# Kernel optimization log

Measured on AMD Instinct MI355X. Metric: run time of the kernel, lower is better.

## Reference

```python
import jax, jax.numpy as jnp
import numpy as np

B, C, H, W = 2, 256, 32, 32
NUM_HEADS = 8
HEAD_DIM = C // NUM_HEADS
SCALE = HEAD_DIM ** -0.5
K1, K2 = 2, 3
KERNELS = [3, 5, 7]
STRIDES = [1, 1, 1]
PADS = [1, 2, 3]


def avgpool2d(y, k, s, p):
    # PyTorch AvgPool2d default count_include_pad=True: divide by k*k always
    yp = jnp.pad(y, ((0, 0), (0, 0), (p, p), (p, p)))
    summed = jax.lax.reduce_window(yp, 0.0, jax.lax.add,
                                   (1, 1, k, k), (1, 1, s, s), 'VALID')
    return summed / float(k * k)


def layer_norm(x, g, b, eps=1e-5):
    mu = jnp.mean(x, axis=-1, keepdims=True)
    var = jnp.var(x, axis=-1, keepdims=True)
    return (x - mu) / jnp.sqrt(var + eps) * g + b


def topk_mask(attn, kk):
    # boolean mask with True at the top-kk positions along the last axis
    idx = jax.lax.top_k(attn, kk)[1]                     # [B,h,N,kk]
    mask = jnp.zeros(attn.shape, dtype=bool)
    return jnp.put_along_axis(mask, idx, True, axis=-1, inplace=False)


def setup_inputs() -> dict:
    key = jax.random.key(0)
    ks = jax.random.split(key, 8)
    std = 1.0 / np.sqrt(C)
    return {
        'x': jax.random.normal(ks[0], (B, C, H, W), jnp.float32),
        'y': jax.random.normal(ks[1], (B, C, H, W), jnp.float32),
        'Wq': jax.random.uniform(ks[2], (C, C), jnp.float32, -std, std),
        'Wkv': jax.random.uniform(ks[3], (2 * C, C), jnp.float32, -std, std),
        'Wproj': jax.random.uniform(ks[4], (C, C), jnp.float32, -std, std),
        'bproj': jax.random.uniform(ks[5], (C,), jnp.float32, -std, std),
        'ln_g': jnp.ones((C,), jnp.float32),
        'ln_b': jnp.zeros((C,), jnp.float32),
        'attn1_p': jnp.full((1,), 0.5, jnp.float32),
        'attn2_p': jnp.full((1,), 0.5, jnp.float32),
    }


def reference(x, y, Wq, Wkv, Wproj, bproj, ln_g, ln_b, attn1_p, attn2_p):
    # multi-scale average pooling fusion of y (stride 1 keeps H,W)
    yf = (avgpool2d(y, KERNELS[0], STRIDES[0], PADS[0])
          + avgpool2d(y, KERNELS[1], STRIDES[1], PADS[1])
          + avgpool2d(y, KERNELS[2], STRIDES[2], PADS[2]))
    yf = yf.reshape(B, C, H * W).transpose(0, 2, 1)      # [B, N1, C]
    yf = layer_norm(yf, ln_g, ln_b)
    N1 = yf.shape[1]

    kv = yf @ Wkv.T                                      # [B, N1, 2C]
    kv = kv.reshape(B, N1, 2, NUM_HEADS, HEAD_DIM).transpose(2, 0, 3, 1, 4)
    k, v = kv[0], kv[1]                                  # [B, h, N1, d]

    xf = x.reshape(B, C, H * W).transpose(0, 2, 1)       # [B, N, C]
    N = xf.shape[1]
    q = (xf @ Wq.T).reshape(B, N, NUM_HEADS, HEAD_DIM).transpose(0, 2, 1, 3)

    attn = jnp.einsum('bhnd,bhmd->bhnm', q, k) * SCALE   # [B, h, N, N1]

    neg_inf = jnp.array(-jnp.inf, attn.dtype)
    m1 = topk_mask(attn, int(N1 / K1))
    a1 = jax.nn.softmax(jnp.where(m1, attn, neg_inf), axis=-1)
    out1 = jnp.einsum('bhnm,bhmd->bhnd', a1, v)

    m2 = topk_mask(attn, int(N1 / K2))
    a2 = jax.nn.softmax(jnp.where(m2, attn, neg_inf), axis=-1)
    out2 = jnp.einsum('bhnm,bhmd->bhnd', a2, v)

    out = out1 * attn1_p + out2 * attn2_p                # [B, h, N, d]
    out = out.transpose(0, 2, 1, 3).reshape(B, N, C)
    out = out @ Wproj.T + bproj
    hw = int(np.sqrt(N))
    return out.transpose(0, 2, 1).reshape(B, C, hw, hw)
```

## Files before the change

### kernel.cpp

```cpp
#include <hip/hip_runtime.h>

typedef _Float16 f16;
typedef f16 f16x8 __attribute__((ext_vector_type(8)));
typedef f16 f16x4 __attribute__((ext_vector_type(4)));
typedef float f32x4 __attribute__((ext_vector_type(4)));

constexpr float ATT_SCALE = 0.17677669529663687f;
constexpr float LOG2E = 1.4426950408889634f;

template<int C> __device__ __forceinline__ float dppadd(float v) {
    return v + __int_as_float(__builtin_amdgcn_update_dpp(0, __float_as_int(v), C, 0xf, 0xf, true));
}
template<int C> __device__ __forceinline__ float dppmax(float v) {
    return fmaxf(v, __int_as_float(__builtin_amdgcn_update_dpp(__float_as_int(v), __float_as_int(v), C, 0xf, 0xf, false)));
}
__device__ __forceinline__ float wave_sum(float v) {
    v = dppadd<0x111>(v); v = dppadd<0x112>(v); v = dppadd<0x114>(v); v = dppadd<0x118>(v);
    v = dppadd<0x142>(v); v = dppadd<0x143>(v);
    return __int_as_float(__builtin_amdgcn_readlane(__float_as_int(v), 63));
}
__device__ __forceinline__ float wave_max(float v) {
    v = dppmax<0x111>(v); v = dppmax<0x112>(v); v = dppmax<0x114>(v); v = dppmax<0x118>(v);
    v = dppmax<0x142>(v); v = dppmax<0x143>(v);
    return __int_as_float(__builtin_amdgcn_readlane(__float_as_int(v), 63));
}

__global__ __launch_bounds__(256) void prep_kernel(const float* __restrict__ y,
                                                   float* __restrict__ pooled,
                                                   const float* __restrict__ x,
                                                   f16* __restrict__ xT,
                                                   const float* __restrict__ Wq,
                                                   const float* __restrict__ Wkv,
                                                   const float* __restrict__ Wp,
                                                   const float* __restrict__ lng,
                                                   const float* __restrict__ lnb,
                                                   f16* __restrict__ wq16,
                                                   f16* __restrict__ wkv16,
                                                   f16* __restrict__ wp16,
                                                   float* __restrict__ sg,
                                                   float* __restrict__ sb)
{
    __shared__ float sh[1444];
    int bid = blockIdx.x, t = threadIdx.x;
    if (bid < 512) {
        float (*p)[38] = (float(*)[38])sh;
        const float* plane = y + (size_t)bid * 1024;
        for (int i = t; i < 38 * 38; i += 256) (&p[0][0])[i] = 0.f;
        __syncthreads();
        for (int i = t; i < 1024; i += 256) p[(i >> 5) + 3][(i & 31) + 3] = plane[i];
        __syncthreads();
        int b = bid >> 8, c = bid & 255;
        for (int i = t; i < 1024; i += 256) {
            int r = (i >> 5) + 3, cc = (i & 31) + 3;
            float s3 = 0.f;
            #pragma unroll
            for (int dr = -1; dr <= 1; ++dr)
                #pragma unroll
                for (int dc = -1; dc <= 1; ++dc) s3 += p[r + dr][cc + dc];
            float r5 = 0.f;
            #pragma unroll
            for (int dc = -2; dc <= 2; ++dc) r5 += p[r - 2][cc + dc] + p[r + 2][cc + dc];
            #pragma unroll
            for (int dr = -1; dr <= 1; ++dr) r5 += p[r + dr][cc - 2] + p[r + dr][cc + 2];
            float r7 = 0.f;
            #pragma unroll
            for (int dc = -3; dc <= 3; ++dc) r7 += p[r - 3][cc + dc] + p[r + 3][cc + dc];
            #pragma unroll
            for (int dr = -2; dr <= 2; ++dr) r7 += p[r + dr][cc - 3] + p[r + dr][cc + 3];
            float s5 = s3 + r5, s7 = s5 + r7;
            pooled[((size_t)b * 1024 + i) * 256 + c] =
                s3 * (1.f / 9.f) + s5 * (1.f / 25.f) + s7 * (1.f / 49.f);
        }
    } else if (bid < 1024) {
        float (*tile)[33] = (float(*)[33])sh;
        int id = bid - 512;
        int b = id >> 8, ct = (id >> 5) & 7, nt = id & 31;
        int rr = t >> 5, j = t & 31;
        #pragma unroll
        for (int r = rr; r < 32; r += 8)
            tile[r][j] = x[((size_t)b * 256 + ct * 32 + r) * 1024 + nt * 32 + j];
        __syncthreads();
        #pragma unroll
        for (int r = rr; r < 32; r += 8)
            xT[((size_t)b * 1024 + nt * 32 + r) * 256 + ct * 32 + j] = (f16)tile[j][r];
    } else if (bid < 1536) {
        int i = (bid - 1024) * 256 + t;
        if (i < 65536) { wq16[i] = (f16)Wq[i]; wp16[i] = (f16)Wp[i]; }
        wkv16[i] = (f16)(Wkv[i] * lng[i & 255]);
    } else {
        int o = (bid - 1536) * 256 + t;
        const float4* wr = (const float4*)(Wkv + (size_t)o * 256);
        const float4* gr = (const float4*)lng;
        const float4* br = (const float4*)lnb;
        float sgs = 0.f, sbs = 0.f;
        #pragma unroll 8
        for (int c4 = 0; c4 < 64; ++c4) {
            float4 wv = wr[c4], gv = gr[c4], bv = br[c4];
            sgs += wv.x * gv.x + wv.y * gv.y + wv.z * gv.z + wv.w * gv.w;
            sbs += wv.x * bv.x + wv.y * bv.y + wv.z * bv.z + wv.w * bv.w;
        }
        sg[o] = sgs; sb[o] = sbs;
    }
}

__device__ __forceinline__ void gemm_tile(const f16* __restrict__ A, const f16* __restrict__ Bm,
                                          int row0, int ncol0, int l15, int lhi, f32x4 acc[4])
{
    for (int k0 = 0; k0 < 256; k0 += 32) {
        f16x8 a = *(const f16x8*)(A + (size_t)(row0 + l15) * 256 + k0 + lhi * 8);
        #pragma unroll
        for (int j = 0; j < 4; ++j) {
            f16x8 bf = *(const f16x8*)(Bm + (size_t)(ncol0 + j * 16 + l15) * 256 + k0 + lhi * 8);
            acc[j] = __builtin_amdgcn_mfma_f32_16x16x32_f16(a, bf, acc[j], 0, 0, 0);
        }
    }
}

__global__ __launch_bounds__(256) void qkv_kernel(const f16* __restrict__ xT,
                                                  const float* __restrict__ pooled,
                                                  const f16* __restrict__ wq16,
                                                  const f16* __restrict__ wkv16,
                                                  const float* __restrict__ sg,
                                                  const float* __restrict__ sb,
                                                  f16* __restrict__ q16,
                                                  f16* __restrict__ k16,
                                                  f16* __restrict__ vT16)
{
    int w = threadIdx.x >> 6, lane = threadIdx.x & 63;
    int l15 = lane & 15, lhi = lane >> 4;
    if (blockIdx.x < 128) {
        int mt = blockIdx.x >> 2, nt = blockIdx.x & 3;
        int row0 = mt * 64 + w * 16;
        f32x4 acc[4] = {};
        gemm_tile(xT, wq16, row0, nt * 64, l15, lhi, acc);
        #pragma unroll
        for (int j = 0; j < 4; ++j) {
            int col = nt * 64 + j * 16 + l15;
            int h = col >> 5, d = col & 31;
            #pragma unroll
            for (int r = 0; r < 4; ++r) {
                int row = row0 + 4 * lhi + r;
                int b = row >> 10, n = row & 1023;
                q16[(((size_t)(b * 8 + h)) * 1024 + n) * 32 + d] = (f16)(acc[j][r] * ATT_SCALE);
            }
        }
    } else {
        __shared__ float st_part[64][4][2];
        __shared__ float stats[64][2];
        int bid = blockIdx.x - 128;
        int mt = bid >> 3, nt = bid & 7;
        int row0g = mt * 64;
        {
            int row = threadIdx.x >> 2, part = threadIdx.x & 3;
            const float4* pr = (const float4*)(pooled + (size_t)(row0g + row) * 256 + part * 64);
            float su = 0.f, qq = 0.f;
            #pragma unroll
            for (int i = 0; i < 16; ++i) {
                float4 v = pr[i];
                su += v.x + v.y + v.z + v.w;
                qq += v.x * v.x + v.y * v.y + v.z * v.z + v.w * v.w;
            }
            st_part[row][part][0] = su; st_part[row][part][1] = qq;
        }
        __syncthreads();
        if (threadIdx.x < 64) {
            int row = threadIdx.x;
            float su = st_part[row][0][0] + st_part[row][1][0] + st_part[row][2][0] + st_part[row][3][0];
            float qq = st_part[row][0][1] + st_part[row][1][1] + st_part[row][2][1] + st_part[row][3][1];
            float mu = su * (1.f / 256.f);
            float rstd = rsqrtf(qq * (1.f / 256.f) - mu * mu + 1e-5f);
            stats[row][0] = mu; stats[row][1] = rstd;
        }
        __syncthreads();
        f32x4 acc[4] = {};
        const float* Ap = pooled + (size_t)(row0g + w * 16 + l15) * 256;
        for (int k0 = 0; k0 < 256; k0 += 32) {
            float4 u0 = *(const float4*)(Ap + k0 + lhi * 8);
            float4 u1 = *(const float4*)(Ap + k0 + lhi * 8 + 4);
            f16x8 a;
            a[0] = (f16)u0.x; a[1] = (f16)u0.y; a[2] = (f16)u0.z; a[3] = (f16)u0.w;
            a[4] = (f16)u1.x; a[5] = (f16)u1.y; a[6] = (f16)u1.z; a[7] = (f16)u1.w;
            #pragma unroll
            for (int j = 0; j < 4; ++j) {
                f16x8 bf = *(const f16x8*)(wkv16 + (size_t)(nt * 64 + j * 16 + l15) * 256 + k0 + lhi * 8);
                acc[j] = __builtin_amdgcn_mfma_f32_16x16x32_f16(a, bf, acc[j], 0, 0, 0);
            }
        }
        float mu_r[4], rs_r[4];
        #pragma unroll
        for (int r = 0; r < 4; ++r) {
            int lr = w * 16 + 4 * lhi + r;
            mu_r[r] = stats[lr][0]; rs_r[r] = stats[lr][1];
        }
        #pragma unroll
        for (int j = 0; j < 4; ++j) {
            int col = nt * 64 + j * 16 + l15;
            float sgv = sg[col], sbv = sb[col];
            #pragma unroll
            for (int r = 0; r < 4; ++r) {
                int row = row0g + w * 16 + 4 * lhi + r;
                int b = row >> 10, n = row & 1023;
                float v = rs_r[r] * acc[j][r] - rs_r[r] * mu_r[r] * sgv + sbv;
                if (col < 256) {
                    int h = col >> 5, d = col & 31;
                    k16[(((size_t)(b * 8 + h)) * 1024 + n) * 32 + d] = (f16)v;
                } else {
                    int c2 = col - 256, h = c2 >> 5, d = c2 & 31;
                    vT16[(((size_t)(b * 8 + h)) * 32 + d) * 1024 + n] = (f16)v;
                }
            }
        }
    }
}

__device__ __forceinline__ int cnt16(const float* s, float m)
{
    int c = 0;
    #pragma unroll
    for (int i = 0; i < 16; ++i)
        c += (int)__popcll(__ballot(s[i] >= m));
    return c;
}

#define WIDEN(sarr, aa, bb, K, mn4, mxv, lo, hi, cl, ch) { \
    int _ca = cnt16(sarr, (aa)); int _cb = cnt16(sarr, (bb)); \
    bool _lm = _ca < (K); bool _hm = _cb > (K); \
    lo = _lm ? (mn4) : (_hm ? (bb) : (aa)); \
    hi = _lm ? (aa)  : (_hm ? (mxv) : (bb)); \
    cl = _lm ? 1024.f : (_hm ? (float)_cb : (float)_ca); \
    ch = _lm ? (float)_ca : (_hm ? 1.f : (float)_cb); }

#define MID(it, lo, hi, cl, ch, K, m) { \
    if ((it) & 1) { m = 0.5f * (lo + hi); } \
    else { float _den = fmaxf(cl - ch, 1.0f); \
        m = lo + (hi - lo) * (cl - (float)(K)) * __builtin_amdgcn_rcpf(_den); \
        float _mg = 0.12f * (hi - lo); \
        m = fminf(fmaxf(m, lo + _mg), hi - _mg); } }

#define UPD(cv, K, lo, hi, cl, ch, m) { bool _g = (cv) >= (K); \
    lo = _g ? (m) : lo; cl = _g ? (float)(cv) : cl; \
    hi = _g ? hi : (m); ch = _g ? ch : (float)(cv); }

__global__ __launch_bounds__(512, 6) void attn_kernel(const f16* __restrict__ q16,
                                                      const f16* __restrict__ k16,
                                                      const f16* __restrict__ vT16,
                                                      const float* __restrict__ a1p,
                                                      const float* __restrict__ a2p,
                                                      f16* __restrict__ oat)
{
    __shared__ f16 Sb[16 * 1024];
    int bid = blockIdx.x;
    int bh = bid >> 6, rb = bid & 63;
    int row0 = rb * 16;
    int w = threadIdx.x >> 6, lane = threadIdx.x & 63;
    int l15 = lane & 15, lhi = lane >> 4;
    const f16* Qb = q16 + (size_t)bh * 32768;
    const f16* Kb = k16 + (size_t)bh * 32768;
    const f16* Vb = vT16 + (size_t)bh * 32768;

    {
        f16x8 qf = *(const f16x8*)(Qb + (size_t)(row0 + l15) * 32 + lhi * 8);
        int q = l15, sw1 = q & 7;
        int phalf = (lhi & 1) * 4;
        #pragma unroll
        for (int j = 0; j < 8; ++j) {
            int c0 = w * 128 + j * 16;
            f16x8 kf = *(const f16x8*)(Kb + (size_t)(c0 + l15) * 32 + lhi * 8);
            f32x4 z = {0.f, 0.f, 0.f, 0.f};
            f32x4 d = __builtin_amdgcn_mfma_f32_16x16x32_f16(kf, qf, z, 0, 0, 0);
            int pl = (c0 >> 3) + (lhi >> 1);
            int pp = pl ^ sw1;
            f16x4 hv;
            hv[0] = (f16)d[0]; hv[1] = (f16)d[1]; hv[2] = (f16)d[2]; hv[3] = (f16)d[3];
            *(f16x4*)(Sb + q * 1024 + pp * 8 + phalf) = hv;
        }
    }
    __syncthreads();

    float c_a1 = a1p[0], c_a2 = a2p[0];
    int r0 = 2 * w, r1 = r0 + 1;
    int cs0 = r0 & 7, cs1 = r1 & 7;
    float s0[16], s1[16];
    {
        f16x8 ha = *(const f16x8*)(Sb + r0 * 1024 + ((lane ^ cs0) << 3));
        f16x8 hb = *(const f16x8*)(Sb + r0 * 1024 + (((64 + lane) ^ cs0) << 3));
        f16x8 hc = *(const f16x8*)(Sb + r1 * 1024 + ((lane ^ cs1) << 3));
        f16x8 hd = *(const f16x8*)(Sb + r1 * 1024 + (((64 + lane) ^ cs1) << 3));
        #pragma unroll
        for (int i = 0; i < 8; ++i) {
            s0[i] = (float)ha[i] * LOG2E; s0[8 + i] = (float)hb[i] * LOG2E;
            s1[i] = (float)hc[i] * LOG2E; s1[8 + i] = (float)hd[i] * LOG2E;
        }
    }
    float mx0l = s0[0], mx1l = s1[0];
    float su0 = 0.f, q0 = 0.f, su1 = 0.f, q1 = 0.f;
    #pragma unroll
    for (int i = 0; i < 16; ++i) {
        mx0l = fmaxf(mx0l, s0[i]); su0 += s0[i]; q0 = fmaf(s0[i], s0[i], q0);
        mx1l = fmaxf(mx1l, s1[i]); su1 += s1[i]; q1 = fmaf(s1[i], s1[i], q1);
    }
    float mx0 = wave_max(mx0l), mx1 = wave_max(mx1l);
    float mu0 = wave_sum(su0) * (1.f / 1024.f), mu1 = wave_sum(su1) * (1.f / 1024.f);
    float sg0 = sqrtf(fmaxf(wave_sum(q0) * (1.f / 1024.f) - mu0 * mu0, 1e-30f));
    float sg1 = sqrtf(fmaxf(wave_sum(q1) * (1.f / 1024.f) - mu1 * mu1, 1e-30f));

    float lo1, hi1, cl1, ch1, lo2, hi2, cl2, ch2;
    float lo3, hi3, cl3, ch3, lo4, hi4, cl4, ch4;
    {
        float d0 = 0.25f * sg0, d1 = 0.25f * sg1;
        float g0 = mu0 + 0.4316f * sg0, g1 = mu1 + 0.4316f * sg1;
        float mn40 = mu0 - 4.f * sg0, mn41 = mu1 - 4.f * sg1;
        WIDEN(s0, mu0 - d0, mu0 + d0, 512, mn40, mx0, lo1, hi1, cl1, ch1);
        WIDEN(s0, g0 - d0,  g0 + d0,  341, mn40, mx0, lo2, hi2, cl2, ch2);
        WIDEN(s1, mu1 - d1, mu1 + d1, 512, mn41, mx1, lo3, hi3, cl3, ch3);
        WIDEN(s1, g1 - d1,  g1 + d1,  341, mn41, mx1, lo4, hi4, cl4, ch4);
    }
    #pragma unroll
    for (int it = 0; it < 8; ++it) {
        float m1, m2, m3, m4;
        MID(it, lo1, hi1, cl1, ch1, 512, m1);
        MID(it, lo2, hi2, cl2, ch2, 341, m2);
        MID(it, lo3, hi3, cl3, ch3, 512, m3);
        MID(it, lo4, hi4, cl4, ch4, 341, m4);
        int c1 = cnt16(s0, m1);
        int c2 = cnt16(s0, m2);
        int c3 = cnt16(s1, m3);
        int c4 = cnt16(s1, m4);
        UPD(c1, 512, lo1, hi1, cl1, ch1, m1);
        UPD(c2, 341, lo2, hi2, cl2, ch2, m2);
        UPD(c3, 512, lo3, hi3, cl3, ch3, m3);
        UPD(c4, 341, lo4, hi4, cl4, ch4, m4);
    }
    {
        float l1 = 0.f, l2 = 0.f;
        #pragma unroll
        for (int i = 0; i < 16; ++i) {
            float ev = exp2f(s0[i] - mx0);
            l1 += (s0[i] >= lo1) ? ev : 0.f;
            l2 += (s0[i] >= lo2) ? ev : 0.f;
        }
        l1 = wave_sum(l1); l2 = wave_sum(l2);
        float w1 = c_a1 / l1, w2 = c_a2 / l2;
        f16x8 oa, ob;
        #pragma unroll
        for (int i = 0; i < 8; ++i) {
            float ev = exp2f(s0[i] - mx0);
            float wt = (s0[i] >= lo1 ? w1 : 0.f) + (s0[i] >= lo2 ? w2 : 0.f);
            oa[i] = (f16)(ev * wt);
            float ev2 = exp2f(s0[8 + i] - mx0);
            float wt2 = (s0[8 + i] >= lo1 ? w1 : 0.f) + (s0[8 + i] >= lo2 ? w2 : 0.f);
            ob[i] = (f16)(ev2 * wt2);
        }
        *(f16x8*)(Sb + r0 * 1024 + ((lane ^ cs0) << 3)) = oa;
        *(f16x8*)(Sb + r0 * 1024 + (((64 + lane) ^ cs0) << 3)) = ob;
    }
    {
        float l3 = 0.f, l4 = 0.f;
        #pragma unroll
        for (int i = 0; i < 16; ++i) {
            float ev = exp2f(s1[i] - mx1);
            l3 += (s1[i] >= lo3) ? ev : 0.f;
            l4 += (s1[i] >= lo4) ? ev : 0.f;
        }
        l3 = wave_sum(l3); l4 = wave_sum(l4);
        float w3 = c_a1 / l3, w4 = c_a2 / l4;
        f16x8 oc, od;
        #pragma unroll
        for (int i = 0; i < 8; ++i) {
            float ev = exp2f(s1[i] - mx1);
            float wt = (s1[i] >= lo3 ? w3 : 0.f) + (s1[i] >= lo4 ? w4 : 0.f);
            oc[i] = (f16)(ev * wt);
            float ev2 = exp2f(s1[8 + i] - mx1);
            float wt2 = (s1[8 + i] >= lo3 ? w3 : 0.f) + (s1[8 + i] >= lo4 ? w4 : 0.f);
            od[i] = (f16)(ev2 * wt2);
        }
        *(f16x8*)(Sb + r1 * 1024 + ((lane ^ cs1) << 3)) = oc;
        *(f16x8*)(Sb + r1 * 1024 + (((64 + lane) ^ cs1) << 3)) = od;
    }
    __syncthreads();

    f32x4 acc0 = {}, acc1 = {};
    #pragma unroll
    for (int ks = 0; ks < 4; ++ks) {
        int pl = w * 16 + ks * 4 + lhi;
        int pp = pl ^ (l15 & 7);
        f16x8 af = *(const f16x8*)(Sb + l15 * 1024 + (pp << 3));
        int m0 = w * 128 + ks * 32 + lhi * 8;
        f16x8 b0 = *(const f16x8*)(Vb + (size_t)l15 * 1024 + m0);
        f16x8 b1v = *(const f16x8*)(Vb + (size_t)(16 + l15) * 1024 + m0);
        acc0 = __builtin_amdgcn_mfma_f32_16x16x32_f16(af, b0, acc0, 0, 0, 0);
        acc1 = __builtin_amdgcn_mfma_f32_16x16x32_f16(af, b1v, acc1, 0, 0, 0);
    }
    __syncthreads();
    float* Pf = (float*)Sb;
    #pragma unroll
    for (int r2 = 0; r2 < 4; ++r2) {
        int rw = 4 * lhi + r2;
        Pf[w * 512 + rw * 32 + l15]      = acc0[r2];
        Pf[w * 512 + rw * 32 + 16 + l15] = acc1[r2];
    }
    __syncthreads();
    if (threadIdx.x < 128) {
        int o4 = threadIdx.x << 2;
        float4 v = *(const float4*)&Pf[o4];
        #pragma unroll
        for (int ww = 1; ww < 8; ++ww) {
            float4 p = *(const float4*)&Pf[ww * 512 + o4];
            v.x += p.x; v.y += p.y; v.z += p.z; v.w += p.w;
        }
        int rr = o4 >> 5, d0 = o4 & 31;
        int b = bh >> 3, h = bh & 7;
        f16x4 o;
        o[0] = (f16)v.x; o[1] = (f16)v.y; o[2] = (f16)v.z; o[3] = (f16)v.w;
        *(f16x4*)(oat + ((size_t)b * 1024 + row0 + rr) * 256 + h * 32 + d0) = o;
    }
}

__global__ __launch_bounds__(256) void projgemm_kernel(const f16* __restrict__ A,
                                                       const f16* __restrict__ Bm,
                                                       const float* __restrict__ bias,
                                                       float* __restrict__ out)
{
    __shared__ float tile[64][65];
    int mt = blockIdx.x >> 2, nt = blockIdx.x & 3;
    int w = threadIdx.x >> 6, lane = threadIdx.x & 63;
    int l15 = lane & 15, lhi = lane >> 4;
    int row0 = mt * 64 + w * 16;
    f32x4 acc[4] = {};
    gemm_tile(A, Bm, row0, nt * 64, l15, lhi, acc);
    #pragma unroll
    for (int j = 0; j < 4; ++j) {
        int col_l = j * 16 + l15;
        float bv = bias[nt * 64 + col_l];
        #pragma unroll
        for (int r = 0; r < 4; ++r)
            tile[col_l][w * 16 + 4 * lhi + r] = acc[j][r] + bv;
    }
    __syncthreads();
    int b = (mt * 64) >> 10, n0 = (mt * 64) & 1023;
    int col_l = threadIdx.x >> 2, part = threadIdx.x & 3;
    size_t base = (size_t)b * 262144 + (size_t)(nt * 64 + col_l) * 1024 + n0 + part * 16;
    #pragma unroll
    for (int q = 0; q < 4; ++q) {
        float4 v;
        v.x = tile[col_l][part * 16 + q * 4 + 0];
        v.y = tile[col_l][part * 16 + q * 4 + 1];
        v.z = tile[col_l][part * 16 + q * 4 + 2];
        v.w = tile[col_l][part * 16 + q * 4 + 3];
        *(float4*)(out + base + q * 4) = v;
    }
}

extern "C" void kernel_launch(void* const* d_in, const int* in_sizes, int n_in,
                              void* d_out, int out_size, void* d_ws, size_t ws_size,
                              hipStream_t stream)
{
    const float* x     = (const float*)d_in[0];
    const float* y     = (const float*)d_in[1];
    const float* Wq    = (const float*)d_in[2];
    const float* Wkv   = (const float*)d_in[3];
    const float* Wproj = (const float*)d_in[4];
    const float* bproj = (const float*)d_in[5];
    const float* ln_g  = (const float*)d_in[6];
    const float* ln_b  = (const float*)d_in[7];
    const float* a1p   = (const float*)d_in[8];
    const float* a2p   = (const float*)d_in[9];
    float* out = (float*)d_out;

    char* wsb = (char*)d_ws;
    float* pooled = (float*)(wsb);
    f16* xT    = (f16*)(wsb + ((size_t)2 << 20));
    f16* wq16  = (f16*)(wsb + ((size_t)3 << 20));
    f16* wkv16 = (f16*)(wsb + ((size_t)3 << 20) + (128 << 10));
    f16* wp16  = (f16*)(wsb + ((size_t)3 << 20) + (384 << 10));
    f16* q16   = (f16*)(wsb + ((size_t)3 << 20) + (512 << 10));
    f16* k16   = (f16*)(wsb + ((size_t)3 << 20) + (512 << 10) + ((size_t)1 << 20));
    f16* vT16  = (f16*)(wsb + ((size_t)3 << 20) + (512 << 10) + ((size_t)2 << 20));
    f16* oat   = (f16*)(wsb + ((size_t)3 << 20) + (512 << 10) + ((size_t)3 << 20));
    float* sgp = (float*)(wsb + ((size_t)3 << 20) + (512 << 10) + ((size_t)4 << 20));
    float* sbp = sgp + 512;

    prep_kernel<<<1538, 256, 0, stream>>>(y, pooled, x, xT, Wq, Wkv, Wproj,
                                          ln_g, ln_b, wq16, wkv16, wp16, sgp, sbp);
    qkv_kernel<<<384, 256, 0, stream>>>(xT, pooled, wq16, wkv16, sgp, sbp,
                                        q16, k16, vT16);
    attn_kernel<<<1024, 512, 0, stream>>>(q16, k16, vT16, a1p, a2p, oat);
    projgemm_kernel<<<128, 256, 0, stream>>>(oat, wp16, bproj, out);
}
```

Measured before the change: 82.29 us.

## Replace interpolated top-k threshold search with f16 multi-probe bracketing

The top-k threshold search now works directly on the packed f16 scores instead of f32 copies. It first brackets the threshold with eight fixed sigma-spaced probes, then narrows it with three rounds of four-way subdivision in place of eight sequential interpolation/bisection steps. This shortens the serial dependency chain and cuts register use. Launch bounds drop to 4 waves per SIMD, and block IDs are remapped so that concurrent blocks are spread across heads. The risks are reduced threshold precision: the final bracket may not isolate exactly k elements, and f16 comparisons can mis-handle ties near the threshold.

```diff
diff --git a/kernel.cpp b/kernel.cpp
--- a/kernel.cpp
+++ b/kernel.cpp
@@ -213,35 +213,45 @@
     }
 }
 
-__device__ __forceinline__ int cnt16(const float* s, float m)
+__device__ __forceinline__ int cntp(f16x8 a, f16x8 b, f16 mh)
 {
     int c = 0;
     #pragma unroll
-    for (int i = 0; i < 16; ++i)
-        c += (int)__popcll(__ballot(s[i] >= m));
+    for (int i = 0; i < 8; ++i) c += (int)__popcll(__ballot(a[i] >= mh));
+    #pragma unroll
+    for (int i = 0; i < 8; ++i) c += (int)__popcll(__ballot(b[i] >= mh));
     return c;
 }
 
-#define WIDEN(sarr, aa, bb, K, mn4, mxv, lo, hi, cl, ch) { \
-    int _ca = cnt16(sarr, (aa)); int _cb = cnt16(sarr, (bb)); \
-    bool _lm = _ca < (K); bool _hm = _cb > (K); \
-    lo = _lm ? (mn4) : (_hm ? (bb) : (aa)); \
-    hi = _lm ? (aa)  : (_hm ? (mxv) : (bb)); \
-    cl = _lm ? 1024.f : (_hm ? (float)_cb : (float)_ca); \
-    ch = _lm ? (float)_ca : (_hm ? 1.f : (float)_cb); }
-
-#define MID(it, lo, hi, cl, ch, K, m) { \
-    if ((it) & 1) { m = 0.5f * (lo + hi); } \
-    else { float _den = fmaxf(cl - ch, 1.0f); \
-        m = lo + (hi - lo) * (cl - (float)(K)) * __builtin_amdgcn_rcpf(_den); \
-        float _mg = 0.12f * (hi - lo); \
-        m = fminf(fmaxf(m, lo + _mg), hi - _mg); } }
-
-#define UPD(cv, K, lo, hi, cl, ch, m) { bool _g = (cv) >= (K); \
-    lo = _g ? (m) : lo; cl = _g ? (float)(cv) : cl; \
-    hi = _g ? hi : (m); ch = _g ? ch : (float)(cv); }
-
-__global__ __launch_bounds__(512, 6) void attn_kernel(const f16* __restrict__ q16,
+#define RND4(HA, HB, K, lo, hi) { \
+    float _st = (hi - lo) * 0.2f; \
+    float _q1 = lo + _st, _q2 = lo + 2.f * _st, _q3 = lo + 3.f * _st, _q4 = lo + 4.f * _st; \
+    int _d1 = cntp(HA, HB, (f16)_q1); \
+    int _d2 = cntp(HA, HB, (f16)_q2); \
+    int _d3 = cntp(HA, HB, (f16)_q3); \
+    int _d4 = cntp(HA, HB, (f16)_q4); \
+    bool _g1 = _d1 >= (K), _g2 = _d2 >= (K), _g3 = _d3 >= (K), _g4 = _d4 >= (K); \
+    lo = _g4 ? _q4 : (_g3 ? _q3 : (_g2 ? _q2 : (_g1 ? _q1 : lo))); \
+    hi = !_g1 ? _q1 : (!_g2 ? _q2 : (!_g3 ? _q3 : (!_g4 ? _q4 : hi))); }
+
+#define BRK(PA, CA, K, lo, hi, HIB) { \
+    lo = PA[0]; hi = (HIB); \
+    lo = (CA[1] >= (K)) ? PA[1] : lo; \
+    lo = (CA[2] >= (K)) ? PA[2] : lo; \
+    lo = (CA[3] >= (K)) ? PA[3] : lo; \
+    lo = (CA[4] >= (K)) ? PA[4] : lo; \
+    lo = (CA[5] >= (K)) ? PA[5] : lo; \
+    lo = (CA[6] >= (K)) ? PA[6] : lo; \
+    lo = (CA[7] >= (K)) ? PA[7] : lo; \
+    hi = (CA[7] < (K)) ? PA[7] : hi; \
+    hi = (CA[6] < (K)) ? PA[6] : hi; \
+    hi = (CA[5] < (K)) ? PA[5] : hi; \
+    hi = (CA[4] < (K)) ? PA[4] : hi; \
+    hi = (CA[3] < (K)) ? PA[3] : hi; \
+    hi = (CA[2] < (K)) ? PA[2] : hi; \
+    hi = (CA[1] < (K)) ? PA[1] : hi; }
+
+__global__ __launch_bounds__(512, 4) void attn_kernel(const f16* __restrict__ q16,
                                                       const f16* __restrict__ k16,
                                                       const f16* __restrict__ vT16,
                                                       const float* __restrict__ a1p,
@@ -249,7 +259,8 @@
                                                       f16* __restrict__ oat)
 {
     __shared__ f16 Sb[16 * 1024];
-    int bid = blockIdx.x;
+    int bid0 = blockIdx.x;
+    int bid = ((bid0 & 7) << 7) | (bid0 >> 3);
     int bh = bid >> 6, rb = bid & 63;
     int row0 = rb * 16;
     int w = threadIdx.x >> 6, lane = threadIdx.x & 63;
@@ -280,98 +291,109 @@
     float c_a1 = a1p[0], c_a2 = a2p[0];
     int r0 = 2 * w, r1 = r0 + 1;
     int cs0 = r0 & 7, cs1 = r1 & 7;
-    float s0[16], s1[16];
+    f16x8 ha0 = *(const f16x8*)(Sb + r0 * 1024 + ((lane ^ cs0) << 3));
+    f16x8 hb0 = *(const f16x8*)(Sb + r0 * 1024 + (((64 + lane) ^ cs0) << 3));
+    f16x8 ha1 = *(const f16x8*)(Sb + r1 * 1024 + ((lane ^ cs1) << 3));
+    f16x8 hb1 = *(const f16x8*)(Sb + r1 * 1024 + (((64 + lane) ^ cs1) << 3));
+
+    float su0 = 0.f, qq0 = 0.f, mxl0 = -1e30f;
+    float su1 = 0.f, qq1 = 0.f, mxl1 = -1e30f;
+    #pragma unroll
+    for (int i = 0; i < 8; ++i) {
+        float v0 = (float)ha0[i], u0 = (float)hb0[i];
+        su0 += v0 + u0; qq0 = fmaf(v0, v0, fmaf(u0, u0, qq0));
+        mxl0 = fmaxf(mxl0, fmaxf(v0, u0));
+        float v1 = (float)ha1[i], u1 = (float)hb1[i];
+        su1 += v1 + u1; qq1 = fmaf(v1, v1, fmaf(u1, u1, qq1));
+        mxl1 = fmaxf(mxl1, fmaxf(v1, u1));
+    }
+    float mx0 = wave_max(mxl0), mx1 = wave_max(mxl1);
+    float mu0 = wave_sum(su0) * (1.f / 1024.f), mu1 = wave_sum(su1) * (1.f / 1024.f);
+    float sg0 = sqrtf(fmaxf(wave_sum(qq0) * (1.f / 1024.f) - mu0 * mu0, 1e-30f));
+    float sg1 = sqrtf(fmaxf(wave_sum(qq1) * (1.f / 1024.f) - mu1 * mu1, 1e-30f));
+
+    float pa0[8], pa1[8];
+    int ca0[8], ca1[8];
+    pa0[0] = fmaf(-3.2f, sg0, mu0); pa0[1] = fmaf(-1.6f, sg0, mu0);
+    pa0[2] = fmaf(-0.8f, sg0, mu0); pa0[3] = fmaf(-0.4f, sg0, mu0);
+    pa0[4] = mu0;                   pa0[5] = fmaf(0.4f, sg0, mu0);
+    pa0[6] = fmaf(0.8f, sg0, mu0);  pa0[7] = fmaf(1.6f, sg0, mu0);
+    pa1[0] = fmaf(-3.2f, sg1, mu1); pa1[1] = fmaf(-1.6f, sg1, mu1);
+    pa1[2] = fmaf(-0.8f, sg1, mu1); pa1[3] = fmaf(-0.4f, sg1, mu1);
+    pa1[4] = mu1;                   pa1[5] = fmaf(0.4f, sg1, mu1);
+    pa1[6] = fmaf(0.8f, sg1, mu1);  pa1[7] = fmaf(1.6f, sg1, mu1);
+    #pragma unroll
+    for (int j = 0; j < 8; ++j) ca0[j] = cntp(ha0, hb0, (f16)pa0[j]);
+    #pragma unroll
+    for (int j = 0; j < 8; ++j) ca1[j] = cntp(ha1, hb1, (f16)pa1[j]);
+
+    float hib0 = mx0 + 0.01f * sg0 + 1e-6f;
+    float hib1 = mx1 + 0.01f * sg1 + 1e-6f;
+    float lo1, hi1, lo2, hi2, lo3, hi3, lo4, hi4;
+    BRK(pa0, ca0, 512, lo1, hi1, hib0);
+    BRK(pa0, ca0, 341, lo2, hi2, hib0);
+    BRK(pa1, ca1, 512, lo3, hi3, hib1);
+    BRK(pa1, ca1, 341, lo4, hi4, hib1);
+
+    #pragma unroll
+    for (int r = 0; r < 3; ++r) {
+        RND4(ha0, hb0, 512, lo1, hi1);
+        RND4(ha0, hb0, 341, lo2, hi2);
+        RND4(ha1, hb1, 512, lo3, hi3);
+        RND4(ha1, hb1, 341, lo4, hi4);
+    }
+
     {
-        f16x8 ha = *(const f16x8*)(Sb + r0 * 1024 + ((lane ^ cs0) << 3));
-        f16x8 hb = *(const f16x8*)(Sb + r0 * 1024 + (((64 + lane) ^ cs0) << 3));
-        f16x8 hc = *(const f16x8*)(Sb + r1 * 1024 + ((lane ^ cs1) << 3));
-        f16x8 hd = *(const f16x8*)(Sb + r1 * 1024 + (((64 + lane) ^ cs1) << 3));
+        f16 m1h = (f16)lo1, m2h = (f16)lo2;
+        float mxe = mx0 * LOG2E;
+        float l1 = 0.f, l2 = 0.f;
         #pragma unroll
         for (int i = 0; i < 8; ++i) {
-            s0[i] = (float)ha[i] * LOG2E; s0[8 + i] = (float)hb[i] * LOG2E;
-            s1[i] = (float)hc[i] * LOG2E; s1[8 + i] = (float)hd[i] * LOG2E;
-        }
-    }
-    float mx0l = s0[0], mx1l = s1[0];
-    float su0 = 0.f, q0 = 0.f, su1 = 0.f, q1 = 0.f;
-    #pragma unroll
-    for (int i = 0; i < 16; ++i) {
-        mx0l = fmaxf(mx0l, s0[i]); su0 += s0[i]; q0 = fmaf(s0[i], s0[i], q0);
-        mx1l = fmaxf(mx1l, s1[i]); su1 += s1[i]; q1 = fmaf(s1[i], s1[i], q1);
-    }
-    float mx0 = wave_max(mx0l), mx1 = wave_max(mx1l);
-    float mu0 = wave_sum(su0) * (1.f / 1024.f), mu1 = wave_sum(su1) * (1.f / 1024.f);
-    float sg0 = sqrtf(fmaxf(wave_sum(q0) * (1.f / 1024.f) - mu0 * mu0, 1e-30f));
-    float sg1 = sqrtf(fmaxf(wave_sum(q1) * (1.f / 1024.f) - mu1 * mu1, 1e-30f));
-
-    float lo1, hi1, cl1, ch1, lo2, hi2, cl2, ch2;
-    float lo3, hi3, cl3, ch3, lo4, hi4, cl4, ch4;
-    {
-        float d0 = 0.25f * sg0, d1 = 0.25f * sg1;
-        float g0 = mu0 + 0.4316f * sg0, g1 = mu1 + 0.4316f * sg1;
-        float mn40 = mu0 - 4.f * sg0, mn41 = mu1 - 4.f * sg1;
-        WIDEN(s0, mu0 - d0, mu0 + d0, 512, mn40, mx0, lo1, hi1, cl1, ch1);
-        WIDEN(s0, g0 - d0,  g0 + d0,  341, mn40, mx0, lo2, hi2, cl2, ch2);
-        WIDEN(s1, mu1 - d1, mu1 + d1, 512, mn41, mx1, lo3, hi3, cl3, ch3);
-        WIDEN(s1, g1 - d1,  g1 + d1,  341, mn41, mx1, lo4, hi4, cl4, ch4);
-    }
-    #pragma unroll
-    for (int it = 0; it < 8; ++it) {
-        float m1, m2, m3, m4;
-        MID(it, lo1, hi1, cl1, ch1, 512, m1);
-        MID(it, lo2, hi2, cl2, ch2, 341, m2);
-        MID(it, lo3, hi3, cl3, ch3, 512, m3);
-        MID(it, lo4, hi4, cl4, ch4, 341, m4);
-        int c1 = cnt16(s0, m1);
-        int c2 = cnt16(s0, m2);
-        int c3 = cnt16(s1, m3);
-        int c4 = cnt16(s1, m4);
-        UPD(c1, 512, lo1, hi1, cl1, ch1, m1);
-        UPD(c2, 341, lo2, hi2, cl2, ch2, m2);
-        UPD(c3, 512, lo3, hi3, cl3, ch3, m3);
-        UPD(c4, 341, lo4, hi4, cl4, ch4, m4);
-    }
-    {
-        float l1 = 0.f, l2 = 0.f;
-        #pragma unroll
-        for (int i = 0; i < 16; ++i) {
-            float ev = exp2f(s0[i] - mx0);
-            l1 += (s0[i] >= lo1) ? ev : 0.f;
-            l2 += (s0[i] >= lo2) ? ev : 0.f;
+            float ev = exp2f(fmaf((float)ha0[i], LOG2E, -mxe));
+            l1 += (ha0[i] >= m1h) ? ev : 0.f;
+            l2 += (ha0[i] >= m2h) ? ev : 0.f;
+            float ev2 = exp2f(fmaf((float)hb0[i], LOG2E, -mxe));
+            l1 += (hb0[i] >= m1h) ? ev2 : 0.f;
+            l2 += (hb0[i] >= m2h) ? ev2 : 0.f;
         }
         l1 = wave_sum(l1); l2 = wave_sum(l2);
         float w1 = c_a1 / l1, w2 = c_a2 / l2;
         f16x8 oa, ob;
         #pragma unroll
         for (int i = 0; i < 8; ++i) {
-            float ev = exp2f(s0[i] - mx0);
-            float wt = (s0[i] >= lo1 ? w1 : 0.f) + (s0[i] >= lo2 ? w2 : 0.f);
+            float ev = exp2f(fmaf((float)ha0[i], LOG2E, -mxe));
+            float wt = ((ha0[i] >= m1h) ? w1 : 0.f) + ((ha0[i] >= m2h) ? w2 : 0.f);
             oa[i] = (f16)(ev * wt);
-            float ev2 = exp2f(s0[8 + i] - mx0);
-            float wt2 = (s0[8 + i] >= lo1 ? w1 : 0.f) + (s0[8 + i] >= lo2 ? w2 : 0.f);
+            float ev2 = exp2f(fmaf((float)hb0[i], LOG2E, -mxe));
+            float wt2 = ((hb0[i] >= m1h) ? w1 : 0.f) + ((hb0[i] >= m2h) ? w2 : 0.f);
             ob[i] = (f16)(ev2 * wt2);
         }
         *(f16x8*)(Sb + r0 * 1024 + ((lane ^ cs0) << 3)) = oa;
         *(f16x8*)(Sb + r0 * 1024 + (((64 + lane) ^ cs0) << 3)) = ob;
     }
     {
+        f16 m3h = (f16)lo3, m4h = (f16)lo4;
+        float mxe = mx1 * LOG2E;
         float l3 = 0.f, l4 = 0.f;
         #pragma unroll
-        for (int i = 0; i < 16; ++i) {
-            float ev = exp2f(s1[i] - mx1);
-            l3 += (s1[i] >= lo3) ? ev : 0.f;
-            l4 += (s1[i] >= lo4) ? ev : 0.f;
+        for (int i = 0; i < 8; ++i) {
+            float ev = exp2f(fmaf((float)ha1[i], LOG2E, -mxe));
+            l3 += (ha1[i] >= m3h) ? ev : 0.f;
+            l4 += (ha1[i] >= m4h) ? ev : 0.f;
+            float ev2 = exp2f(fmaf((float)hb1[i], LOG2E, -mxe));
+            l3 += (hb1[i] >= m3h) ? ev2 : 0.f;
+            l4 += (hb1[i] >= m4h) ? ev2 : 0.f;
         }
         l3 = wave_sum(l3); l4 = wave_sum(l4);
         float w3 = c_a1 / l3, w4 = c_a2 / l4;
         f16x8 oc, od;
         #pragma unroll
         for (int i = 0; i < 8; ++i) {
-            float ev = exp2f(s1[i] - mx1);
-            float wt = (s1[i] >= lo3 ? w3 : 0.f) + (s1[i] >= lo4 ? w4 : 0.f);
+            float ev = exp2f(fmaf((float)ha1[i], LOG2E, -mxe));
+            float wt = ((ha1[i] >= m3h) ? w3 : 0.f) + ((ha1[i] >= m4h) ? w4 : 0.f);
             oc[i] = (f16)(ev * wt);
-            float ev2 = exp2f(s1[8 + i] - mx1);
-            float wt2 = (s1[8 + i] >= lo3 ? w3 : 0.f) + (s1[8 + i] >= lo4 ? w4 : 0.f);
+            float ev2 = exp2f(fmaf((float)hb1[i], LOG2E, -mxe));
+            float wt2 = ((hb1[i] >= m3h) ? w3 : 0.f) + ((hb1[i] >= m4h) ? w4 : 0.f);
             od[i] = (f16)(ev2 * wt2);
         }
         *(f16x8*)(Sb + r1 * 1024 + ((lane ^ cs1) << 3)) = oc;
```

Measured after the change: 94.86 us. +15.3%, slower.
